# Kernel tuning notes

Measured on AMD Instinct MI355X. Metric: run time of the kernel, lower is better.

Reference implementation:

```python
import jax, jax.numpy as jnp
import numpy as np

CONTEXT_LENGTHS = [1, 3, 5, 7]
PADS = [(f - 1) // 2 for f in CONTEXT_LENGTHS]  # p(f) for odd f
B, H, L, DK = 2, 8, 1024, 64
C = H * DK  # conv channels = d_k * n_heads


def _conv1d(x, w, b, pad):
    # x: (b, C, L), w: (C, C, f), b: (C,) -- torch Conv1d semantics
    y = jax.lax.conv_general_dilated(
        x, w, window_strides=(1,), padding=[(pad, pad)],
        dimension_numbers=("NCH", "OIH", "NCH"))
    return y + b[None, :, None]


def _plane(a, w, b, pad, out_len):
    # Faithful to: conv(a.reshape(b, h*d_k, -1)).reshape(b, h, -1, d_k)[:, :, :out_len, :]
    bsz, h, l, d = a.shape
    y = _conv1d(a.reshape(bsz, h * d, l), w, b, pad)
    return y.reshape(bsz, h, -1, d)[:, :, :out_len, :]


def setup_inputs() -> dict:
    key = jax.random.key(0)
    ks = jax.random.split(key, 12)
    inp = {
        "Q": jax.random.normal(ks[0], (B, H, L, DK), jnp.float32),
        "K": jax.random.normal(ks[1], (B, H, L, DK), jnp.float32),
        "V": jax.random.normal(ks[2], (B, H, L, DK), jnp.float32),
        # causal mask: True = masked
        "attn_mask": jnp.broadcast_to(
            jnp.triu(jnp.ones((L, L), jnp.bool_), k=1), (B, H, L, L)),
    }
    for i, f in enumerate(CONTEXT_LENGTHS):
        scale = 1.0 / np.sqrt(C * f)
        inp[f"conv_w{i}"] = jax.random.normal(ks[3 + i], (C, C, f), jnp.float32) * scale
        inp[f"conv_b{i}"] = jax.random.normal(ks[7 + i], (C,), jnp.float32) * scale
    return inp


def reference(Q, K, V, attn_mask,
              conv_w0, conv_b0, conv_w1, conv_b1,
              conv_w2, conv_b2, conv_w3, conv_b3):
    ws = [conv_w0, conv_w1, conv_w2, conv_w3]
    bs = [conv_b0, conv_b1, conv_b2, conv_b3]
    b, h, l, d_k = Q.shape
    l_k = K.shape[2]
    p = len(CONTEXT_LENGTHS)
    Q_l = [_plane(Q, ws[i], bs[i], PADS[i], l) for i in range(p)]
    K_l = [_plane(K, ws[i], bs[i], PADS[i], l_k) for i in range(p)]
    # replicate torch.cat(dim=0).reshape(b, h, p, l, d) exactly (row-major)
    Q_p = jnp.concatenate(Q_l, axis=0).reshape(b, h, p, l, d_k)
    K_p = jnp.concatenate(K_l, axis=0).reshape(b, h, p, l_k, d_k)
    scores = jnp.einsum("bhpqd,bhpkd->bhpqk", Q_p, K_p) / np.sqrt(d_k).astype(np.float32)
    scores = jnp.where(attn_mask[:, :, None, :, :], jnp.float32(-1e9), scores)
    attn = jax.nn.softmax(scores, axis=-1)
    attn = jnp.max(attn, axis=2)  # max over planes -> (b,h,q,k)
    context = jnp.einsum("bhqk,bhkd->bhqd", attn, V)
    return (context, attn)
```

## Files before the change

kernel.cpp:

```cpp
#include <hip/hip_runtime.h>
#include <math.h>

#define C_CH 512
#define L_SEQ 1024
#define DK 64
#define NP 4

typedef __attribute__((ext_vector_type(8))) short short8;
typedef __attribute__((ext_vector_type(4))) float f32x4;

__device__ __forceinline__ unsigned short f2bf(float f) {
    union { float f; unsigned u; } v; v.f = f;
    unsigned u = v.u;
    u += 0x7FFFu + ((u >> 16) & 1u);
    return (unsigned short)(u >> 16);
}

__global__ __launch_bounds__(256)
void prep_w_kernel(const float* __restrict__ w0, const float* __restrict__ w1,
                   const float* __restrict__ w2, const float* __restrict__ w3,
                   unsigned short* __restrict__ Wb) {
    int tg = blockIdx.y;
    int plane, t;
    if (tg < 1)      { plane = 0; t = tg; }
    else if (tg < 4) { plane = 1; t = tg - 1; }
    else if (tg < 9) { plane = 2; t = tg - 4; }
    else             { plane = 3; t = tg - 9; }
    const float* W = (plane == 0) ? w0 : (plane == 1) ? w1 : (plane == 2) ? w2 : w3;
    const int f = (plane == 0) ? 1 : (plane == 1) ? 3 : (plane == 2) ? 5 : 7;

    int co = blockIdx.x * 32 + (threadIdx.x >> 3);
    int c8 = threadIdx.x & 7;
    for (int it = 0; it < 8; it++) {
        int ci = c8 * 8 + it * 64;
        unsigned short o[8];
#pragma unroll
        for (int j = 0; j < 8; j++)
            o[j] = f2bf(W[(size_t)(co * C_CH + ci + j) * f + t]);
        *(short8*)&Wb[((size_t)tg * C_CH + co) * C_CH + ci] = *(short8*)o;
    }
}

__global__ __launch_bounds__(256)
void prep_x_kernel(const float* __restrict__ Qin, const float* __restrict__ Kin,
                   unsigned short* __restrict__ Xt) {
    int tb = blockIdx.z;
    int tensor = tb >> 1, b = tb & 1;
    const float* X = (tensor ? Kin : Qin) + (size_t)b * C_CH * L_SEQ;
    unsigned short* O = Xt + (size_t)tb * 1032 * C_CH;

    int pos0 = blockIdx.x * 64;
    int ci0  = blockIdx.y * 64;
    int tid = threadIdx.x;

    __shared__ float tile[64][65];
    int tx = tid & 15, ty = tid >> 4;
#pragma unroll
    for (int rr = 0; rr < 4; rr++) {
        int ci_l = ty + rr * 16;
        float4 v = *(const float4*)&X[(size_t)(ci0 + ci_l) * L_SEQ + pos0 + tx * 4];
        tile[tx * 4 + 0][ci_l] = v.x;
        tile[tx * 4 + 1][ci_l] = v.y;
        tile[tx * 4 + 2][ci_l] = v.z;
        tile[tx * 4 + 3][ci_l] = v.w;
    }
    __syncthreads();
#pragma unroll
    for (int pp = 0; pp < 2; pp++) {
        int pos_l = (tid >> 3) + pp * 32;
        int cg = (tid & 7) * 8;
        unsigned short o[8];
#pragma unroll
        for (int j = 0; j < 8; j++) o[j] = f2bf(tile[pos_l][cg + j]);
        *(short8*)&O[(size_t)(pos0 + pos_l + 4) * C_CH + ci0 + cg] = *(short8*)o;
    }
    if (blockIdx.x == 0) {
        int r = tid >> 6, cc = tid & 63;
        O[(size_t)r * C_CH + ci0 + cc] = 0;
    }
    if (blockIdx.x == 15) {
        int r = tid >> 6, cc = tid & 63;
        O[(size_t)(1028 + r) * C_CH + ci0 + cc] = 0;
    }
}

__global__ __launch_bounds__(256)
void conv_mfma_kernel(const unsigned short* __restrict__ Xt,
                      const unsigned short* __restrict__ Wb,
                      const float* __restrict__ b0, const float* __restrict__ b1,
                      const float* __restrict__ b2, const float* __restrict__ b3,
                      unsigned short* __restrict__ Qp, unsigned short* __restrict__ Kp) {
    const int fs[4]   = {1, 3, 5, 7};
    const int toff[4] = {0, 1, 4, 9};
    int combo  = blockIdx.x;
    int b      = combo & 1;
    int plane  = (combo >> 1) & 3;
    int tensor = combo >> 3;
    const int f   = fs[plane];
    const int pad = (f - 1) >> 1;
    const float* bias = (plane == 0) ? b0 : (plane == 1) ? b1 : (plane == 2) ? b2 : b3;
    unsigned short* Out = tensor ? Kp : Qp;
    const unsigned short* Xbase = Xt + (size_t)(tensor * 2 + b) * 1032 * C_CH;

    int pos0 = blockIdx.y * 128;
    int co0  = blockIdx.z * 128;

    __shared__ __align__(16) unsigned short As[128 * 40];
    __shared__ __align__(16) unsigned short Bs[128 * 40];

    int tid  = threadIdx.x;
    int w    = tid >> 6;
    int lane = tid & 63;
    int l15  = lane & 15;
    int quad = lane >> 4;
    int wm = (w & 1) * 64;
    int wn = (w >> 1) * 64;

    int rowS = tid >> 2;
    int cS   = tid & 3;

    f32x4 acc[4][4];
#pragma unroll
    for (int mi = 0; mi < 4; mi++)
#pragma unroll
        for (int ni = 0; ni < 4; ni++) acc[mi][ni] = (f32x4){0.f, 0.f, 0.f, 0.f};

    for (int t = 0; t < f; t++) {
        const unsigned short* Wsl = Wb + ((size_t)(toff[plane] + t) * C_CH + co0) * C_CH;
        const unsigned short* Xsl = Xbase + (size_t)(pos0 + t - pad + 4) * C_CH;
        for (int cc = 0; cc < 16; cc++) {
            int kb = cc * 32;
            __syncthreads();
#pragma unroll
            for (int rep = 0; rep < 2; rep++) {
                int row = rowS + rep * 64;
                short8 va = *(const short8*)&Wsl[(size_t)row * C_CH + kb + cS * 8];
                *(short8*)&As[row * 40 + cS * 8] = va;
                short8 vb = *(const short8*)&Xsl[(size_t)row * C_CH + kb + cS * 8];
                *(short8*)&Bs[row * 40 + cS * 8] = vb;
            }
            __syncthreads();

            short8 af[4], bf[4];
#pragma unroll
            for (int mi = 0; mi < 4; mi++)
                af[mi] = *(const short8*)&As[(wm + mi * 16 + l15) * 40 + quad * 8];
#pragma unroll
            for (int ni = 0; ni < 4; ni++)
                bf[ni] = *(const short8*)&Bs[(wn + ni * 16 + l15) * 40 + quad * 8];
#pragma unroll
            for (int mi = 0; mi < 4; mi++)
#pragma unroll
                for (int ni = 0; ni < 4; ni++)
                    acc[mi][ni] = __builtin_amdgcn_mfma_f32_16x16x32_bf16(
                        af[mi], bf[ni], acc[mi][ni], 0, 0, 0);
        }
    }

#pragma unroll
    for (int mi = 0; mi < 4; mi++)
#pragma unroll
        for (int r = 0; r < 4; r++) {
            int co_l = wm + mi * 16 + quad * 4 + r;
            int co = co0 + co_l;
            int h = co >> 6, cl = co & 63;
            float bv = bias[co];
            size_t sbase = (size_t)((b * 8 + h) * NP + plane) * L_SEQ * DK;
#pragma unroll
            for (int ni = 0; ni < 4; ni++) {
                int pos = pos0 + wn + ni * 16 + l15;
                int l = cl * 16 + (pos >> 6);
                int d = pos & 63;
                Out[sbase + (size_t)l * DK + d] = f2bf(acc[mi][ni][r] + bv);
            }
        }
}

__global__ __launch_bounds__(256)
void attn_stats_kernel(const unsigned short* __restrict__ Qb,
                       const unsigned short* __restrict__ Kb,
                       float2* __restrict__ pstats) {
    int kc = blockIdx.x, qt = blockIdx.y, bh = blockIdx.z;
    int tid = threadIdx.x;
    size_t pbase = ((size_t)(bh * 16 + qt) * 4 + kc) * (NP * 64);

    if (kc * 4 > qt) {
        pstats[pbase + tid] = make_float2(-1e30f, 0.f);
        return;
    }

    int q0 = qt * 64;
    int b2 = bh >> 3, h2 = bh & 7;
    int plane  = b2 * 2 + (h2 >> 2);
    int b_orig = (h2 >> 1) & 1;
    int h_base = (h2 & 1) * 4;
    int w = tid >> 6, lane = tid & 63, l15 = lane & 15, quad = lane >> 4;

    const unsigned short* kbase[NP];
    short8 qa[NP][2];
#pragma unroll
    for (int p = 0; p < NP; p++) {
        size_t slice = (size_t)((b_orig * 8 + h_base + p) * NP + plane);
        kbase[p] = Kb + slice * L_SEQ * DK;
        const unsigned short* qrow =
            Qb + (slice * L_SEQ + (size_t)(q0 + w * 16 + l15)) * DK + quad * 8;
        qa[p][0] = *(const short8*)(qrow);
        qa[p][1] = *(const short8*)(qrow + 32);
    }

    float m[NP][4], l[NP][4];
#pragma unroll
    for (int p = 0; p < NP; p++)
        for (int r = 0; r < 4; r++) { m[p][r] = -1e30f; l[p][r] = 0.f; }

    int kt1 = min(kc * 4 + 3, qt);
    for (int kt = kc * 4; kt <= kt1; kt++) {
        int k0 = kt * 64;
        bool diag = (kt == qt);
#pragma unroll
        for (int p = 0; p < NP; p++) {
            f32x4 c[4];
#pragma unroll
            for (int s = 0; s < 4; s++) {
                const unsigned short* kr =
                    kbase[p] + (size_t)(k0 + s * 16 + l15) * DK + quad * 8;
                short8 kb0 = *(const short8*)(kr);
                short8 kb1 = *(const short8*)(kr + 32);
                f32x4 acc = {0.f, 0.f, 0.f, 0.f};
                acc = __builtin_amdgcn_mfma_f32_16x16x32_bf16(qa[p][0], kb0, acc, 0, 0, 0);
                acc = __builtin_amdgcn_mfma_f32_16x16x32_bf16(qa[p][1], kb1, acc, 0, 0, 0);
                c[s] = acc;
            }
#pragma unroll
            for (int r = 0; r < 4; r++) {
                int row_local = quad * 4 + r + w * 16;
                float sv[4];
                float tm = -1e30f;
#pragma unroll
                for (int s = 0; s < 4; s++) {
                    float x = c[s][r] * 0.125f;
                    if (diag && (s * 16 + l15 > row_local)) x = -1e30f;
                    sv[s] = x;
                    tm = fmaxf(tm, x);
                }
                float mo = m[p][r];
                float mn = fmaxf(mo, tm);
                float fac = __expf(mo - mn);
                float add = __expf(sv[0] - mn) + __expf(sv[1] - mn) +
                            __expf(sv[2] - mn) + __expf(sv[3] - mn);
                m[p][r] = mn;
                l[p][r] = l[p][r] * fac + add;
            }
        }
    }

#pragma unroll
    for (int p = 0; p < NP; p++)
#pragma unroll
        for (int r = 0; r < 4; r++) {
            float mm = m[p][r];
            mm = fmaxf(mm, __shfl_xor(mm, 1));
            mm = fmaxf(mm, __shfl_xor(mm, 2));
            mm = fmaxf(mm, __shfl_xor(mm, 4));
            mm = fmaxf(mm, __shfl_xor(mm, 8));
            float ll = l[p][r] * __expf(m[p][r] - mm);
            ll += __shfl_xor(ll, 1);
            ll += __shfl_xor(ll, 2);
            ll += __shfl_xor(ll, 4);
            ll += __shfl_xor(ll, 8);
            if (l15 == 0)
                pstats[pbase + p * 64 + (w * 16 + quad * 4 + r)] = make_float2(mm, ll);
        }
}

__global__ __launch_bounds__(256)
void attn_combine_kernel(const float2* __restrict__ pstats,
                         float2* __restrict__ fstats,
                         float* __restrict__ out_ctx) {
    int qt = blockIdx.x, bh = blockIdx.y;
    int tid = threadIdx.x;
    size_t base = ((size_t)(bh * 16 + qt) * 4) * (NP * 64);

    float2 s[4];
    float m = -1e30f;
#pragma unroll
    for (int kc = 0; kc < 4; kc++) {
        s[kc] = pstats[base + (size_t)kc * (NP * 64) + tid];
        m = fmaxf(m, s[kc].x);
    }
    float l = 0.f;
#pragma unroll
    for (int kc = 0; kc < 4; kc++)
        l += s[kc].y * __expf(s[kc].x - m);
    fstats[(size_t)(bh * 16 + qt) * (NP * 64) + tid] = make_float2(m, 1.f / l);

    int r = tid >> 2, c = (tid & 3) * 16;
    float4 z = make_float4(0.f, 0.f, 0.f, 0.f);
    size_t cbase = ((size_t)bh * L_SEQ + qt * 64 + r) * DK + c;
#pragma unroll
    for (int j = 0; j < 4; j++)
        *(float4*)&out_ctx[cbase + j * 4] = z;
}

__global__ __launch_bounds__(256)
void attn_apply_kernel(const unsigned short* __restrict__ Qb,
                       const unsigned short* __restrict__ Kb,
                       const float* __restrict__ V,
                       const float2* __restrict__ fstats,
                       float* __restrict__ out_ctx, float* __restrict__ out_attn) {
    int kt = blockIdx.x, qt = blockIdx.y, bh = blockIdx.z;
    int tid = threadIdx.x;
    int q0 = qt * 64, k0 = kt * 64;

    if (kt > qt) {
        float4 z = make_float4(0.f, 0.f, 0.f, 0.f);
        size_t base = ((size_t)bh * L_SEQ + q0 + (tid >> 2)) * L_SEQ + k0 + (tid & 3) * 16;
#pragma unroll
        for (int j = 0; j < 4; j++)
            *(float4*)&out_attn[base + j * 4] = z;
        return;
    }

    int b2 = bh >> 3, h2 = bh & 7;
    int plane  = b2 * 2 + (h2 >> 2);
    int b_orig = (h2 >> 1) & 1;
    int h_base = (h2 & 1) * 4;
    int w = tid >> 6, lane = tid & 63, l15 = lane & 15, quad = lane >> 4;
    bool diag = (kt == qt);

    __shared__ float2 sstats[NP * 64];
    __shared__ __align__(16) unsigned short ast[64 * 80];
    __shared__ __align__(16) unsigned short vts[64 * 80];

    sstats[tid] = fstats[(size_t)(bh * 16 + qt) * (NP * 64) + tid];

    const unsigned short* kbase[NP];
    short8 qa[NP][2];
#pragma unroll
    for (int p = 0; p < NP; p++) {
        size_t slice = (size_t)((b_orig * 8 + h_base + p) * NP + plane);
        kbase[p] = Kb + slice * L_SEQ * DK;
        const unsigned short* qrow =
            Qb + (slice * L_SEQ + (size_t)(q0 + w * 16 + l15)) * DK + quad * 8;
        qa[p][0] = *(const short8*)(qrow);
        qa[p][1] = *(const short8*)(qrow + 32);
    }

    {
        int kl = tid >> 2, db = (tid & 3) * 16;
        const float* vr = V + ((size_t)bh * L_SEQ + k0 + kl) * DK + db;
        float vv[16];
        *(float4*)&vv[0]  = *(const float4*)(vr);
        *(float4*)&vv[4]  = *(const float4*)(vr + 4);
        *(float4*)&vv[8]  = *(const float4*)(vr + 8);
        *(float4*)&vv[12] = *(const float4*)(vr + 12);
#pragma unroll
        for (int j = 0; j < 16; j++)
            vts[(db + j) * 80 + kl] = f2bf(vv[j]);
    }
    __syncthreads();

    float aval[4][4];
#pragma unroll
    for (int s = 0; s < 4; s++)
        for (int r = 0; r < 4; r++) aval[s][r] = 0.f;

#pragma unroll
    for (int p = 0; p < NP; p++) {
        f32x4 c[4];
#pragma unroll
        for (int s = 0; s < 4; s++) {
            const unsigned short* kr =
                kbase[p] + (size_t)(k0 + s * 16 + l15) * DK + quad * 8;
            short8 kb0 = *(const short8*)(kr);
            short8 kb1 = *(const short8*)(kr + 32);
            f32x4 acc = {0.f, 0.f, 0.f, 0.f};
            acc = __builtin_amdgcn_mfma_f32_16x16x32_bf16(qa[p][0], kb0, acc, 0, 0, 0);
            acc = __builtin_amdgcn_mfma_f32_16x16x32_bf16(qa[p][1], kb1, acc, 0, 0, 0);
            c[s] = acc;
        }
#pragma unroll
        for (int r = 0; r < 4; r++) {
            int row_local = quad * 4 + r + w * 16;
            float2 st = sstats[p * 64 + row_local];
#pragma unroll
            for (int s = 0; s < 4; s++) {
                float x = c[s][r] * 0.125f;
                if (diag && (s * 16 + l15 > row_local)) x = -1e30f;
                float e = __expf(x - st.x) * st.y;
                aval[s][r] = fmaxf(aval[s][r], e);
            }
        }
    }

#pragma unroll
    for (int s = 0; s < 4; s++)
#pragma unroll
        for (int r = 0; r < 4; r++) {
            int qloc = w * 16 + quad * 4 + r;
            int kg   = k0 + s * 16 + l15;
            out_attn[((size_t)bh * L_SEQ + q0 + qloc) * L_SEQ + kg] = aval[s][r];
            ast[qloc * 80 + s * 16 + l15] = f2bf(aval[s][r]);
        }
    __syncthreads();

    f32x4 ctxc[4];
#pragma unroll
    for (int ds = 0; ds < 4; ds++) ctxc[ds] = (f32x4){0.f, 0.f, 0.f, 0.f};
    short8 af0 = *(const short8*)&ast[(w * 16 + l15) * 80 + quad * 8];
    short8 af1 = *(const short8*)&ast[(w * 16 + l15) * 80 + 32 + quad * 8];
#pragma unroll
    for (int ds = 0; ds < 4; ds++) {
        short8 bf0 = *(const short8*)&vts[(ds * 16 + l15) * 80 + quad * 8];
        short8 bf1 = *(const short8*)&vts[(ds * 16 + l15) * 80 + 32 + quad * 8];
        ctxc[ds] = __builtin_amdgcn_mfma_f32_16x16x32_bf16(af0, bf0, ctxc[ds], 0, 0, 0);
        ctxc[ds] = __builtin_amdgcn_mfma_f32_16x16x32_bf16(af1, bf1, ctxc[ds], 0, 0, 0);
    }

#pragma unroll
    for (int ds = 0; ds < 4; ds++)
#pragma unroll
        for (int r = 0; r < 4; r++) {
            int qg = q0 + w * 16 + quad * 4 + r;
            unsafeAtomicAdd(&out_ctx[((size_t)bh * L_SEQ + qg) * DK + ds * 16 + l15],
                            ctxc[ds][r]);
        }
}

extern "C" void kernel_launch(void* const* d_in, const int* in_sizes, int n_in,
                              void* d_out, int out_size, void* d_ws, size_t ws_size,
                              hipStream_t stream) {
    const float* Q  = (const float*)d_in[0];
    const float* K  = (const float*)d_in[1];
    const float* V  = (const float*)d_in[2];
    const float* w0 = (const float*)d_in[4];
    const float* b0 = (const float*)d_in[5];
    const float* w1 = (const float*)d_in[6];
    const float* b1 = (const float*)d_in[7];
    const float* w2 = (const float*)d_in[8];
    const float* b2 = (const float*)d_in[9];
    const float* w3 = (const float*)d_in[10];
    const float* b3 = (const float*)d_in[11];

    char* ws = (char*)d_ws;
    unsigned short* Wb = (unsigned short*)(ws);
    unsigned short* Xt = (unsigned short*)(ws + 8388608);
    unsigned short* Qp = (unsigned short*)(ws + 12615680);
    unsigned short* Kp = (unsigned short*)(ws + 21004288);
    float2* pstats = (float2*)(ws + 8388608);
    float2* fstats = (float2*)(ws + 8388608 + 2097152);

    float* out_ctx  = (float*)d_out;
    float* out_attn = out_ctx + 1048576;

    prep_w_kernel<<<dim3(16, 16), 256, 0, stream>>>(w0, w1, w2, w3, Wb);
    prep_x_kernel<<<dim3(16, 8, 4), 256, 0, stream>>>(Q, K, Xt);
    conv_mfma_kernel<<<dim3(16, 8, 4), 256, 0, stream>>>(Xt, Wb, b0, b1, b2, b3, Qp, Kp);
    attn_stats_kernel<<<dim3(4, 16, 16), 256, 0, stream>>>(Qp, Kp, pstats);
    attn_combine_kernel<<<dim3(16, 16), 256, 0, stream>>>(pstats, fstats, out_ctx);
    attn_apply_kernel<<<dim3(16, 16, 16), 256, 0, stream>>>(Qp, Kp, V, fstats,
                                                            out_ctx, out_attn);
}
```

Before: 393.6 us.

## Pair conv planes per block, prefetch with swizzled LDS, drop softmax max tracking

```diff
diff --git a/kernel.cpp b/kernel.cpp
--- a/kernel.cpp
+++ b/kernel.cpp
@@ -5,6 +5,7 @@
 #define L_SEQ 1024
 #define DK 64
 #define NP 4
+#define SC2 0.1803368801111f
 
 typedef __attribute__((ext_vector_type(8))) short short8;
 typedef __attribute__((ext_vector_type(4))) float f32x4;
@@ -85,28 +86,25 @@
 }
 
 __global__ __launch_bounds__(256)
-void conv_mfma_kernel(const unsigned short* __restrict__ Xt,
+void conv_pair_kernel(const unsigned short* __restrict__ Xt,
                       const unsigned short* __restrict__ Wb,
                       const float* __restrict__ b0, const float* __restrict__ b1,
                       const float* __restrict__ b2, const float* __restrict__ b3,
                       unsigned short* __restrict__ Qp, unsigned short* __restrict__ Kp) {
     const int fs[4]   = {1, 3, 5, 7};
     const int toff[4] = {0, 1, 4, 9};
-    int combo  = blockIdx.x;
-    int b      = combo & 1;
-    int plane  = (combo >> 1) & 3;
-    int tensor = combo >> 3;
-    const int f   = fs[plane];
-    const int pad = (f - 1) >> 1;
-    const float* bias = (plane == 0) ? b0 : (plane == 1) ? b1 : (plane == 2) ? b2 : b3;
+    int blk = blockIdx.x;
+    int cls = blk >> 7;
+    int idx = blk & 127;
+    int co0  = (idx & 3) * 128;
+    int pos0 = ((idx >> 2) & 7) * 128;
+    int tb   = idx >> 5;
+    int tensor = tb >> 1, b = tb & 1;
     unsigned short* Out = tensor ? Kp : Qp;
-    const unsigned short* Xbase = Xt + (size_t)(tensor * 2 + b) * 1032 * C_CH;
-
-    int pos0 = blockIdx.y * 128;
-    int co0  = blockIdx.z * 128;
-
-    __shared__ __align__(16) unsigned short As[128 * 40];
-    __shared__ __align__(16) unsigned short Bs[128 * 40];
+    const unsigned short* Xbase = Xt + (size_t)tb * 1032 * C_CH;
+
+    __shared__ __align__(16) unsigned short As[4096];
+    __shared__ __align__(16) unsigned short Bs[4096];
 
     int tid  = threadIdx.x;
     int w    = tid >> 6;
@@ -115,39 +113,80 @@
     int quad = lane >> 4;
     int wm = (w & 1) * 64;
     int wn = (w >> 1) * 64;
-
-    int rowS = tid >> 2;
+    int rowL = tid >> 2;
     int cS   = tid & 3;
 
-    f32x4 acc[4][4];
-#pragma unroll
-    for (int mi = 0; mi < 4; mi++)
-#pragma unroll
-        for (int ni = 0; ni < 4; ni++) acc[mi][ni] = (f32x4){0.f, 0.f, 0.f, 0.f};
-
-    for (int t = 0; t < f; t++) {
-        const unsigned short* Wsl = Wb + ((size_t)(toff[plane] + t) * C_CH + co0) * C_CH;
-        const unsigned short* Xsl = Xbase + (size_t)(pos0 + t - pad + 4) * C_CH;
-        for (int cc = 0; cc < 16; cc++) {
-            int kb = cc * 32;
+    int woff[2];
+#pragma unroll
+    for (int rep = 0; rep < 2; rep++) {
+        int r = rowL + rep * 64;
+        int line = r >> 1;
+        int sl = (((r & 1) << 2) | cS) ^ (line & 7);
+        woff[rep] = line * 64 + sl * 8;
+    }
+    int aoff[4], boff[4];
+#pragma unroll
+    for (int mi = 0; mi < 4; mi++) {
+        int r = wm + mi * 16 + l15;
+        int line = r >> 1;
+        aoff[mi] = line * 64 + ((((r & 1) << 2) | quad) ^ (line & 7)) * 8;
+        int r2 = wn + mi * 16 + l15;
+        int line2 = r2 >> 1;
+        boff[mi] = line2 * 64 + ((((r2 & 1) << 2) | quad) ^ (line2 & 7)) * 8;
+    }
+
+    for (int ti = 0; ti < 2; ti++) {
+        int plane = (cls == 0) ? (ti == 0 ? 0 : 3) : (ti == 0 ? 1 : 2);
+        const int f   = fs[plane];
+        const int pad = (f - 1) >> 1;
+        const float* bias = (plane == 0) ? b0 : (plane == 1) ? b1 : (plane == 2) ? b2 : b3;
+        const int n = f * 16;
+
+        f32x4 acc[4][4];
+#pragma unroll
+        for (int mi = 0; mi < 4; mi++)
+#pragma unroll
+            for (int ni = 0; ni < 4; ni++) acc[mi][ni] = (f32x4){0.f, 0.f, 0.f, 0.f};
+
+        short8 pA[2], pB[2];
+        {
+            const unsigned short* Wsl = Wb + ((size_t)toff[plane] * C_CH + co0) * C_CH;
+            const unsigned short* Xsl = Xbase + (size_t)(pos0 - pad + 4) * C_CH;
+#pragma unroll
+            for (int rep = 0; rep < 2; rep++) {
+                int r = rowL + rep * 64;
+                pA[rep] = *(const short8*)&Wsl[(size_t)r * C_CH + cS * 8];
+                pB[rep] = *(const short8*)&Xsl[(size_t)r * C_CH + cS * 8];
+            }
+        }
+
+        for (int it = 0; it < n; it++) {
             __syncthreads();
-#pragma unroll
-            for (int rep = 0; rep < 2; rep++) {
-                int row = rowS + rep * 64;
-                short8 va = *(const short8*)&Wsl[(size_t)row * C_CH + kb + cS * 8];
-                *(short8*)&As[row * 40 + cS * 8] = va;
-                short8 vb = *(const short8*)&Xsl[(size_t)row * C_CH + kb + cS * 8];
-                *(short8*)&Bs[row * 40 + cS * 8] = vb;
-            }
+            *(short8*)&As[woff[0]] = pA[0];
+            *(short8*)&As[woff[1]] = pA[1];
+            *(short8*)&Bs[woff[0]] = pB[0];
+            *(short8*)&Bs[woff[1]] = pB[1];
             __syncthreads();
 
+            if (it + 1 < n) {
+                int t = (it + 1) >> 4, cc = (it + 1) & 15;
+                const unsigned short* Wsl =
+                    Wb + ((size_t)(toff[plane] + t) * C_CH + co0) * C_CH + cc * 32;
+                const unsigned short* Xsl =
+                    Xbase + (size_t)(pos0 + t - pad + 4) * C_CH + cc * 32;
+#pragma unroll
+                for (int rep = 0; rep < 2; rep++) {
+                    int r = rowL + rep * 64;
+                    pA[rep] = *(const short8*)&Wsl[(size_t)r * C_CH + cS * 8];
+                    pB[rep] = *(const short8*)&Xsl[(size_t)r * C_CH + cS * 8];
+                }
+            }
+
             short8 af[4], bf[4];
 #pragma unroll
-            for (int mi = 0; mi < 4; mi++)
-                af[mi] = *(const short8*)&As[(wm + mi * 16 + l15) * 40 + quad * 8];
-#pragma unroll
-            for (int ni = 0; ni < 4; ni++)
-                bf[ni] = *(const short8*)&Bs[(wn + ni * 16 + l15) * 40 + quad * 8];
+            for (int mi = 0; mi < 4; mi++) af[mi] = *(const short8*)&As[aoff[mi]];
+#pragma unroll
+            for (int ni = 0; ni < 4; ni++) bf[ni] = *(const short8*)&Bs[boff[ni]];
 #pragma unroll
             for (int mi = 0; mi < 4; mi++)
 #pragma unroll
@@ -155,39 +194,35 @@
                     acc[mi][ni] = __builtin_amdgcn_mfma_f32_16x16x32_bf16(
                         af[mi], bf[ni], acc[mi][ni], 0, 0, 0);
         }
-    }
-
-#pragma unroll
-    for (int mi = 0; mi < 4; mi++)
-#pragma unroll
-        for (int r = 0; r < 4; r++) {
-            int co_l = wm + mi * 16 + quad * 4 + r;
-            int co = co0 + co_l;
-            int h = co >> 6, cl = co & 63;
-            float bv = bias[co];
-            size_t sbase = (size_t)((b * 8 + h) * NP + plane) * L_SEQ * DK;
-#pragma unroll
-            for (int ni = 0; ni < 4; ni++) {
-                int pos = pos0 + wn + ni * 16 + l15;
-                int l = cl * 16 + (pos >> 6);
-                int d = pos & 63;
-                Out[sbase + (size_t)l * DK + d] = f2bf(acc[mi][ni][r] + bv);
-            }
-        }
+
+#pragma unroll
+        for (int mi = 0; mi < 4; mi++)
+#pragma unroll
+            for (int r = 0; r < 4; r++) {
+                int co = co0 + wm + mi * 16 + quad * 4 + r;
+                int h = co >> 6, cl = co & 63;
+                float bv = bias[co];
+                size_t sbase = (size_t)((b * 8 + h) * NP + plane) * L_SEQ * DK;
+#pragma unroll
+                for (int ni = 0; ni < 4; ni++) {
+                    int pos = pos0 + wn + ni * 16 + l15;
+                    int l = cl * 16 + (pos >> 6);
+                    int d = pos & 63;
+                    Out[sbase + (size_t)l * DK + d] = f2bf(acc[mi][ni][r] + bv);
+                }
+            }
+    }
 }
 
 __global__ __launch_bounds__(256)
 void attn_stats_kernel(const unsigned short* __restrict__ Qb,
                        const unsigned short* __restrict__ Kb,
-                       float2* __restrict__ pstats) {
+                       float* __restrict__ pstats) {
     int kc = blockIdx.x, qt = blockIdx.y, bh = blockIdx.z;
     int tid = threadIdx.x;
     size_t pbase = ((size_t)(bh * 16 + qt) * 4 + kc) * (NP * 64);
 
-    if (kc * 4 > qt) {
-        pstats[pbase + tid] = make_float2(-1e30f, 0.f);
-        return;
-    }
+    if (kc * 4 > qt) { pstats[pbase + tid] = 0.f; return; }
 
     int q0 = qt * 64;
     int b2 = bh >> 3, h2 = bh & 7;
@@ -208,10 +243,10 @@
         qa[p][1] = *(const short8*)(qrow + 32);
     }
 
-    float m[NP][4], l[NP][4];
+    float l[NP][4];
 #pragma unroll
     for (int p = 0; p < NP; p++)
-        for (int r = 0; r < 4; r++) { m[p][r] = -1e30f; l[p][r] = 0.f; }
+        for (int r = 0; r < 4; r++) l[p][r] = 0.f;
 
     int kt1 = min(kc * 4 + 3, qt);
     for (int kt = kc * 4; kt <= kt1; kt++) {
@@ -234,22 +269,12 @@
 #pragma unroll
             for (int r = 0; r < 4; r++) {
                 int row_local = quad * 4 + r + w * 16;
-                float sv[4];
-                float tm = -1e30f;
 #pragma unroll
                 for (int s = 0; s < 4; s++) {
-                    float x = c[s][r] * 0.125f;
+                    float x = c[s][r] * SC2;
                     if (diag && (s * 16 + l15 > row_local)) x = -1e30f;
-                    sv[s] = x;
-                    tm = fmaxf(tm, x);
+                    l[p][r] += exp2f(x);
                 }
-                float mo = m[p][r];
-                float mn = fmaxf(mo, tm);
-                float fac = __expf(mo - mn);
-                float add = __expf(sv[0] - mn) + __expf(sv[1] - mn) +
-                            __expf(sv[2] - mn) + __expf(sv[3] - mn);
-                m[p][r] = mn;
-                l[p][r] = l[p][r] * fac + add;
             }
         }
     }
@@ -258,41 +283,29 @@
     for (int p = 0; p < NP; p++)
 #pragma unroll
         for (int r = 0; r < 4; r++) {
-            float mm = m[p][r];
-            mm = fmaxf(mm, __shfl_xor(mm, 1));
-            mm = fmaxf(mm, __shfl_xor(mm, 2));
-            mm = fmaxf(mm, __shfl_xor(mm, 4));
-            mm = fmaxf(mm, __shfl_xor(mm, 8));
-            float ll = l[p][r] * __expf(m[p][r] - mm);
+            float ll = l[p][r];
             ll += __shfl_xor(ll, 1);
             ll += __shfl_xor(ll, 2);
             ll += __shfl_xor(ll, 4);
             ll += __shfl_xor(ll, 8);
             if (l15 == 0)
-                pstats[pbase + p * 64 + (w * 16 + quad * 4 + r)] = make_float2(mm, ll);
-        }
-}
-
-__global__ __launch_bounds__(256)
-void attn_combine_kernel(const float2* __restrict__ pstats,
-                         float2* __restrict__ fstats,
+                pstats[pbase + p * 64 + (w * 16 + quad * 4 + r)] = ll;
+        }
+}
+
+__global__ __launch_bounds__(256)
+void attn_combine_kernel(const float* __restrict__ pstats,
+                         float* __restrict__ fstats,
                          float* __restrict__ out_ctx) {
     int qt = blockIdx.x, bh = blockIdx.y;
     int tid = threadIdx.x;
     size_t base = ((size_t)(bh * 16 + qt) * 4) * (NP * 64);
 
-    float2 s[4];
-    float m = -1e30f;
-#pragma unroll
-    for (int kc = 0; kc < 4; kc++) {
-        s[kc] = pstats[base + (size_t)kc * (NP * 64) + tid];
-        m = fmaxf(m, s[kc].x);
-    }
     float l = 0.f;
 #pragma unroll
     for (int kc = 0; kc < 4; kc++)
-        l += s[kc].y * __expf(s[kc].x - m);
-    fstats[(size_t)(bh * 16 + qt) * (NP * 64) + tid] = make_float2(m, 1.f / l);
+        l += pstats[base + (size_t)kc * (NP * 64) + tid];
+    fstats[(size_t)(bh * 16 + qt) * (NP * 64) + tid] = __log2f(l);
 
     int r = tid >> 2, c = (tid & 3) * 16;
     float4 z = make_float4(0.f, 0.f, 0.f, 0.f);
@@ -306,125 +319,134 @@
 void attn_apply_kernel(const unsigned short* __restrict__ Qb,
                        const unsigned short* __restrict__ Kb,
                        const float* __restrict__ V,
-                       const float2* __restrict__ fstats,
+                       const float* __restrict__ fstats,
                        float* __restrict__ out_ctx, float* __restrict__ out_attn) {
-    int kt = blockIdx.x, qt = blockIdx.y, bh = blockIdx.z;
+    int kc = blockIdx.x, qt = blockIdx.y, bh = blockIdx.z;
     int tid = threadIdx.x;
-    int q0 = qt * 64, k0 = kt * 64;
-
-    if (kt > qt) {
-        float4 z = make_float4(0.f, 0.f, 0.f, 0.f);
-        size_t base = ((size_t)bh * L_SEQ + q0 + (tid >> 2)) * L_SEQ + k0 + (tid & 3) * 16;
-#pragma unroll
-        for (int j = 0; j < 4; j++)
-            *(float4*)&out_attn[base + j * 4] = z;
-        return;
-    }
+    int q0 = qt * 64;
+    bool any = (kc * 4 <= qt);
 
     int b2 = bh >> 3, h2 = bh & 7;
     int plane  = b2 * 2 + (h2 >> 2);
     int b_orig = (h2 >> 1) & 1;
     int h_base = (h2 & 1) * 4;
     int w = tid >> 6, lane = tid & 63, l15 = lane & 15, quad = lane >> 4;
-    bool diag = (kt == qt);
-
-    __shared__ float2 sstats[NP * 64];
+
+    __shared__ float zsm[NP * 64];
     __shared__ __align__(16) unsigned short ast[64 * 80];
     __shared__ __align__(16) unsigned short vts[64 * 80];
 
-    sstats[tid] = fstats[(size_t)(bh * 16 + qt) * (NP * 64) + tid];
-
     const unsigned short* kbase[NP];
     short8 qa[NP][2];
-#pragma unroll
-    for (int p = 0; p < NP; p++) {
-        size_t slice = (size_t)((b_orig * 8 + h_base + p) * NP + plane);
-        kbase[p] = Kb + slice * L_SEQ * DK;
-        const unsigned short* qrow =
-            Qb + (slice * L_SEQ + (size_t)(q0 + w * 16 + l15)) * DK + quad * 8;
-        qa[p][0] = *(const short8*)(qrow);
-        qa[p][1] = *(const short8*)(qrow + 32);
-    }
-
-    {
-        int kl = tid >> 2, db = (tid & 3) * 16;
-        const float* vr = V + ((size_t)bh * L_SEQ + k0 + kl) * DK + db;
-        float vv[16];
-        *(float4*)&vv[0]  = *(const float4*)(vr);
-        *(float4*)&vv[4]  = *(const float4*)(vr + 4);
-        *(float4*)&vv[8]  = *(const float4*)(vr + 8);
-        *(float4*)&vv[12] = *(const float4*)(vr + 12);
-#pragma unroll
-        for (int j = 0; j < 16; j++)
-            vts[(db + j) * 80 + kl] = f2bf(vv[j]);
-    }
-    __syncthreads();
-
-    float aval[4][4];
-#pragma unroll
-    for (int s = 0; s < 4; s++)
-        for (int r = 0; r < 4; r++) aval[s][r] = 0.f;
-
-#pragma unroll
-    for (int p = 0; p < NP; p++) {
-        f32x4 c[4];
-#pragma unroll
-        for (int s = 0; s < 4; s++) {
-            const unsigned short* kr =
-                kbase[p] + (size_t)(k0 + s * 16 + l15) * DK + quad * 8;
-            short8 kb0 = *(const short8*)(kr);
-            short8 kb1 = *(const short8*)(kr + 32);
-            f32x4 acc = {0.f, 0.f, 0.f, 0.f};
-            acc = __builtin_amdgcn_mfma_f32_16x16x32_bf16(qa[p][0], kb0, acc, 0, 0, 0);
-            acc = __builtin_amdgcn_mfma_f32_16x16x32_bf16(qa[p][1], kb1, acc, 0, 0, 0);
-            c[s] = acc;
-        }
-#pragma unroll
-        for (int r = 0; r < 4; r++) {
-            int row_local = quad * 4 + r + w * 16;
-            float2 st = sstats[p * 64 + row_local];
+    if (any) {
+        zsm[tid] = fstats[(size_t)(bh * 16 + qt) * (NP * 64) + tid];
+#pragma unroll
+        for (int p = 0; p < NP; p++) {
+            size_t slice = (size_t)((b_orig * 8 + h_base + p) * NP + plane);
+            kbase[p] = Kb + slice * L_SEQ * DK;
+            const unsigned short* qrow =
+                Qb + (slice * L_SEQ + (size_t)(q0 + w * 16 + l15)) * DK + quad * 8;
+            qa[p][0] = *(const short8*)(qrow);
+            qa[p][1] = *(const short8*)(qrow + 32);
+        }
+    }
+
+    f32x4 ctxc[4];
+#pragma unroll
+    for (int ds = 0; ds < 4; ds++) ctxc[ds] = (f32x4){0.f, 0.f, 0.f, 0.f};
+
+    for (int k4 = 0; k4 < 4; k4++) {
+        int kt = kc * 4 + k4;
+        int k0 = kt * 64;
+
+        if (kt > qt) {
+            float4 z = make_float4(0.f, 0.f, 0.f, 0.f);
+            size_t abase = ((size_t)bh * L_SEQ + q0) * L_SEQ + k0;
+#pragma unroll
+            for (int j = 0; j < 4; j++) {
+                int flat = tid + j * 256;
+                *(float4*)&out_attn[abase + (size_t)(flat >> 4) * L_SEQ + (flat & 15) * 4] = z;
+            }
+            continue;
+        }
+        bool diag = (kt == qt);
+
+        __syncthreads();
+
+        {
+            int kl = tid >> 2, db = (tid & 3) * 16;
+            const float* vr = V + ((size_t)bh * L_SEQ + k0 + kl) * DK + db;
+            float vv[16];
+            *(float4*)&vv[0]  = *(const float4*)(vr);
+            *(float4*)&vv[4]  = *(const float4*)(vr + 4);
+            *(float4*)&vv[8]  = *(const float4*)(vr + 8);
+            *(float4*)&vv[12] = *(const float4*)(vr + 12);
+#pragma unroll
+            for (int j = 0; j < 16; j++)
+                vts[(db + j) * 80 + kl] = f2bf(vv[j]);
+        }
+
+        float run[4][4];
+#pragma unroll
+        for (int s = 0; s < 4; s++)
+            for (int r = 0; r < 4; r++) run[s][r] = -1e30f;
+
+#pragma unroll
+        for (int p = 0; p < NP; p++) {
+            f32x4 c[4];
 #pragma unroll
             for (int s = 0; s < 4; s++) {
-                float x = c[s][r] * 0.125f;
-                if (diag && (s * 16 + l15 > row_local)) x = -1e30f;
-                float e = __expf(x - st.x) * st.y;
-                aval[s][r] = fmaxf(aval[s][r], e);
-            }
-        }
-    }
-
-#pragma unroll
-    for (int s = 0; s < 4; s++)
-#pragma unroll
-        for (int r = 0; r < 4; r++) {
-            int qloc = w * 16 + quad * 4 + r;
-            int kg   = k0 + s * 16 + l15;
-            out_attn[((size_t)bh * L_SEQ + q0 + qloc) * L_SEQ + kg] = aval[s][r];
-            ast[qloc * 80 + s * 16 + l15] = f2bf(aval[s][r]);
-        }
-    __syncthreads();
-
-    f32x4 ctxc[4];
-#pragma unroll
-    for (int ds = 0; ds < 4; ds++) ctxc[ds] = (f32x4){0.f, 0.f, 0.f, 0.f};
-    short8 af0 = *(const short8*)&ast[(w * 16 + l15) * 80 + quad * 8];
-    short8 af1 = *(const short8*)&ast[(w * 16 + l15) * 80 + 32 + quad * 8];
-#pragma unroll
-    for (int ds = 0; ds < 4; ds++) {
-        short8 bf0 = *(const short8*)&vts[(ds * 16 + l15) * 80 + quad * 8];
-        short8 bf1 = *(const short8*)&vts[(ds * 16 + l15) * 80 + 32 + quad * 8];
-        ctxc[ds] = __builtin_amdgcn_mfma_f32_16x16x32_bf16(af0, bf0, ctxc[ds], 0, 0, 0);
-        ctxc[ds] = __builtin_amdgcn_mfma_f32_16x16x32_bf16(af1, bf1, ctxc[ds], 0, 0, 0);
-    }
-
-#pragma unroll
-    for (int ds = 0; ds < 4; ds++)
-#pragma unroll
-        for (int r = 0; r < 4; r++) {
-            int qg = q0 + w * 16 + quad * 4 + r;
-            unsafeAtomicAdd(&out_ctx[((size_t)bh * L_SEQ + qg) * DK + ds * 16 + l15],
-                            ctxc[ds][r]);
-        }
+                const unsigned short* kr =
+                    kbase[p] + (size_t)(k0 + s * 16 + l15) * DK + quad * 8;
+                short8 kb0 = *(const short8*)(kr);
+                short8 kb1 = *(const short8*)(kr + 32);
+                f32x4 acc = {0.f, 0.f, 0.f, 0.f};
+                acc = __builtin_amdgcn_mfma_f32_16x16x32_bf16(qa[p][0], kb0, acc, 0, 0, 0);
+                acc = __builtin_amdgcn_mfma_f32_16x16x32_bf16(qa[p][1], kb1, acc, 0, 0, 0);
+                c[s] = acc;
+            }
+#pragma unroll
+            for (int r = 0; r < 4; r++) {
+                float zp = zsm[p * 64 + (quad * 4 + r + w * 16)];
+#pragma unroll
+                for (int s = 0; s < 4; s++)
+                    run[s][r] = fmaxf(run[s][r], c[s][r] * SC2 - zp);
+            }
+        }
+
+#pragma unroll
+        for (int s = 0; s < 4; s++)
+#pragma unroll
+            for (int r = 0; r < 4; r++) {
+                int qloc = w * 16 + quad * 4 + r;
+                bool masked = diag && (s * 16 + l15 > qloc);
+                float a = masked ? 0.f : exp2f(run[s][r]);
+                out_attn[((size_t)bh * L_SEQ + q0 + qloc) * L_SEQ + k0 + s * 16 + l15] = a;
+                ast[qloc * 80 + s * 16 + l15] = f2bf(a);
+            }
+        __syncthreads();
+
+        short8 af0 = *(const short8*)&ast[(w * 16 + l15) * 80 + quad * 8];
+        short8 af1 = *(const short8*)&ast[(w * 16 + l15) * 80 + 32 + quad * 8];
+#pragma unroll
+        for (int ds = 0; ds < 4; ds++) {
+            short8 bf0 = *(const short8*)&vts[(ds * 16 + l15) * 80 + quad * 8];
+            short8 bf1 = *(const short8*)&vts[(ds * 16 + l15) * 80 + 32 + quad * 8];
+            ctxc[ds] = __builtin_amdgcn_mfma_f32_16x16x32_bf16(af0, bf0, ctxc[ds], 0, 0, 0);
+            ctxc[ds] = __builtin_amdgcn_mfma_f32_16x16x32_bf16(af1, bf1, ctxc[ds], 0, 0, 0);
+        }
+    }
+
+    if (any) {
+#pragma unroll
+        for (int ds = 0; ds < 4; ds++)
+#pragma unroll
+            for (int r = 0; r < 4; r++) {
+                int qg = q0 + w * 16 + quad * 4 + r;
+                unsafeAtomicAdd(&out_ctx[((size_t)bh * L_SEQ + qg) * DK + ds * 16 + l15],
+                                ctxc[ds][r]);
+            }
+    }
 }
 
 extern "C" void kernel_launch(void* const* d_in, const int* in_sizes, int n_in,
@@ -447,17 +469,17 @@
     unsigned short* Xt = (unsigned short*)(ws + 8388608);
     unsigned short* Qp = (unsigned short*)(ws + 12615680);
     unsigned short* Kp = (unsigned short*)(ws + 21004288);
-    float2* pstats = (float2*)(ws + 8388608);
-    float2* fstats = (float2*)(ws + 8388608 + 2097152);
+    float* pstats = (float*)(ws + 8388608);
+    float* fstats = (float*)(ws + 8388608 + 1048576);
 
     float* out_ctx  = (float*)d_out;
     float* out_attn = out_ctx + 1048576;
 
     prep_w_kernel<<<dim3(16, 16), 256, 0, stream>>>(w0, w1, w2, w3, Wb);
     prep_x_kernel<<<dim3(16, 8, 4), 256, 0, stream>>>(Q, K, Xt);
-    conv_mfma_kernel<<<dim3(16, 8, 4), 256, 0, stream>>>(Xt, Wb, b0, b1, b2, b3, Qp, Kp);
+    conv_pair_kernel<<<dim3(256), 256, 0, stream>>>(Xt, Wb, b0, b1, b2, b3, Qp, Kp);
     attn_stats_kernel<<<dim3(4, 16, 16), 256, 0, stream>>>(Qp, Kp, pstats);
     attn_combine_kernel<<<dim3(16, 16), 256, 0, stream>>>(pstats, fstats, out_ctx);
-    attn_apply_kernel<<<dim3(16, 16, 16), 256, 0, stream>>>(Qp, Kp, V, fstats,
-                                                            out_ctx, out_attn);
-}
+    attn_apply_kernel<<<dim3(4, 16, 16), 256, 0, stream>>>(Qp, Kp, V, fstats,
+                                                           out_ctx, out_attn);
+}
```

Result: faster. 365.6 us (-7.1%).
